# Kernel optimization log

Measured on AMD Instinct MI355X. Metric: run time of the kernel, lower is better.

The kernel has to match this reference:

```python
import jax, jax.numpy as jnp
import numpy as np

V, H, T = 32000, 768, 32
TYPES, MAX_VISITS, SEGS = 9, 512, 3
B, S = 32, 2048
EPS = 1e-12


def setup_inputs() -> dict:
    key = jax.random.key(0)
    ks = jax.random.split(key, 16)
    input_ids = jax.random.randint(ks[0], (B, S), 0, V)
    type_ids = jax.random.randint(ks[1], (B, S), 0, TYPES)
    time_stamps = jax.random.uniform(ks[2], (B, S), dtype=jnp.float32)
    ages = jax.random.uniform(ks[3], (B, S), dtype=jnp.float32)
    visit_orders = jax.random.randint(ks[4], (B, S), 0, MAX_VISITS)
    visit_segments = jax.random.randint(ks[5], (B, S), 0, SEGS)
    # parameters
    W_word = jax.random.normal(ks[6], (V, H), jnp.float32) * 0.02
    W_word = W_word.at[0].set(0.0)  # padding_idx = 0
    W_type = jax.random.normal(ks[7], (TYPES, H), jnp.float32) * 0.02
    W_order = jax.random.normal(ks[8], (MAX_VISITS, H), jnp.float32) * 0.02
    W_seg = jax.random.normal(ks[9], (SEGS, H), jnp.float32) * 0.02
    time_w = jax.random.normal(ks[10], (1, T), jnp.float32)
    time_phi = jax.random.normal(ks[11], (1, T), jnp.float32)
    age_w = jax.random.normal(ks[12], (1, T), jnp.float32)
    age_phi = jax.random.normal(ks[13], (1, T), jnp.float32)
    lin_W = jax.random.normal(ks[14], (H + 2 * T, H), jnp.float32) * 0.02
    lin_b = jnp.zeros((H,), jnp.float32)
    ln_g = jnp.ones((H,), jnp.float32)
    ln_beta = jnp.zeros((H,), jnp.float32)
    return dict(input_ids=input_ids, type_ids=type_ids, time_stamps=time_stamps,
                ages=ages, visit_orders=visit_orders, visit_segments=visit_segments,
                W_word=W_word, W_type=W_type, W_order=W_order, W_seg=W_seg,
                time_w=time_w, time_phi=time_phi, age_w=age_w, age_phi=age_phi,
                lin_W=lin_W, lin_b=lin_b, ln_g=ln_g, ln_beta=ln_beta)


def _sinusoidal(t, w, phi):
    # t: [B,S]; w,phi: [1,T] -> [B,S,T]
    return jnp.sin(t[..., None] * w + phi)


def reference(input_ids, type_ids, time_stamps, ages, visit_orders, visit_segments,
              W_word, W_type, W_order, W_seg, time_w, time_phi, age_w, age_phi,
              lin_W, lin_b, ln_g, ln_beta):
    word = W_word[input_ids]                       # [B,S,H]
    # time delta embedding (is_time_delta=True)
    dt = jnp.concatenate([time_stamps[:, :1] * 0.0,
                          time_stamps[:, 1:] - time_stamps[:, :-1]], axis=-1)
    time_e = _sinusoidal(dt, time_w, time_phi)     # [B,S,T]
    age_e = _sinusoidal(ages, age_w, age_phi)      # [B,S,T]
    seg_e = W_seg[visit_segments]                  # [B,S,H]
    order_e = W_order[visit_orders]                # [B,S,H]
    type_e = W_type[type_ids]                      # [B,S,H]
    fused = jnp.concatenate([word, time_e, age_e], axis=-1)   # [B,S,H+2T]
    fused = jnp.tanh(fused @ lin_W + lin_b)        # [B,S,H]
    emb = fused + type_e + order_e + seg_e
    # dropout is identity in eval mode; LayerNorm(eps=1e-12)
    mu = jnp.mean(emb, axis=-1, keepdims=True)
    var = jnp.mean(jnp.square(emb - mu), axis=-1, keepdims=True)
    return (emb - mu) * jax.lax.rsqrt(var + EPS) * ln_g + ln_beta
```

## Files before the change

### kernel.cpp

```cpp
#include <hip/hip_runtime.h>
#include <hip/hip_bf16.h>
#include <math.h>
#include <stdint.h>

#define HH 768
#define TT 32
#define KK 832
#define SS 2048
#define NSTEP 26
#define NTOK 65536
#define BM 32

typedef __attribute__((ext_vector_type(4))) float f32x4;
typedef __attribute__((ext_vector_type(8))) short bf16x8;
typedef __attribute__((ext_vector_type(4))) short bf16x4;

__device__ __forceinline__ short f2bf(float f) {
  union { float f; uint32_t u; } v; v.f = f;
  uint32_t u = v.u;
  return (short)((u + 0x7FFFu + ((u >> 16) & 1u)) >> 16);
}

__global__ void transpose_w_kernel(const float* __restrict__ lin_W,
                                   short* __restrict__ bt) {
  int i = blockIdx.x * 256 + threadIdx.x;
  if (i >= HH * KK) return;
  int n = i / KK;
  int k = i - n * KK;
  bt[i] = f2bf(lin_W[(size_t)k * HH + n]);
}

__global__ __launch_bounds__(256) void gather_a_kernel(
    const int* __restrict__ input_ids, const float* __restrict__ ts,
    const float* __restrict__ ages, const float* __restrict__ W_word,
    const float* __restrict__ time_w, const float* __restrict__ time_phi,
    const float* __restrict__ age_w, const float* __restrict__ age_phi,
    short* __restrict__ Aws) {
  const int wave = threadIdx.x >> 6, lane = threadIdx.x & 63;
  const int t = blockIdx.x * 4 + wave;
  if (t >= NTOK) return;
  const float* wrow = W_word + (size_t)input_ids[t] * HH;
  const int s = t & (SS - 1);
  const float dt = (s == 0) ? 0.f : (ts[t] - ts[t - 1]);
  const float age = ages[t];
  short* dst = Aws + (size_t)t * KK;
#pragma unroll
  for (int c2 = 0; c2 < 2; ++c2) {
    int chunk = c2 * 64 + lane;
    if (chunk < 104) {
      int k = chunk * 8;
      bf16x8 v;
      if (k < HH) {
        f32x4 x0 = *(const f32x4*)(wrow + k);
        f32x4 x1 = *(const f32x4*)(wrow + k + 4);
        v[0] = f2bf(x0[0]); v[1] = f2bf(x0[1]); v[2] = f2bf(x0[2]); v[3] = f2bf(x0[3]);
        v[4] = f2bf(x1[0]); v[5] = f2bf(x1[1]); v[6] = f2bf(x1[2]); v[7] = f2bf(x1[3]);
      } else if (k < HH + TT) {
        int j = k - HH;
#pragma unroll
        for (int i = 0; i < 8; ++i)
          v[i] = f2bf(sinf(dt * time_w[j + i] + time_phi[j + i]));
      } else {
        int j = k - HH - TT;
#pragma unroll
        for (int i = 0; i < 8; ++i)
          v[i] = f2bf(sinf(age * age_w[j + i] + age_phi[j + i]));
      }
      *(bf16x8*)(dst + k) = v;
    }
  }
}

__global__ __launch_bounds__(512) void ehr_gemm_kernel(
    const int* __restrict__ type_ids, const int* __restrict__ visit_orders,
    const int* __restrict__ visit_segments, const float* __restrict__ W_type,
    const float* __restrict__ W_order, const float* __restrict__ W_seg,
    const float* __restrict__ lin_b, const float* __restrict__ ln_g,
    const float* __restrict__ ln_beta, const short* __restrict__ Aws,
    const short* __restrict__ Btw, float* __restrict__ out) {
  __shared__ short Bt[HH * 32];
  __shared__ short Atile[BM * 32];
  __shared__ int tyl[BM], orl[BM], sgl[BM];
  __shared__ float redS[4][BM], redQ[4][BM];

  const int tid = threadIdx.x;
  const int t0 = blockIdx.x * BM;
  if (tid < BM) {
    tyl[tid] = type_ids[t0 + tid];
    orl[tid] = visit_orders[t0 + tid];
    sgl[tid] = visit_segments[t0 + tid];
  }
  const int lane = tid & 63, wave = tid >> 6;
  const int wm = wave >> 2, wn = wave & 3;
  const int l15 = lane & 15, l4 = lane >> 4;

  f32x4 acc[12];
#pragma unroll
  for (int nf = 0; nf < 12; ++nf) acc[nf] = (f32x4)(0.0f);

  const size_t a_lane_off = (size_t)l15 * KK + l4 * 8;

  for (int st = 0; st < NSTEP; ++st) {
    const int k0 = st * 32;
    if (wave < 2) {
      const short* src = Aws + (size_t)(t0 + wave * 16) * KK + a_lane_off + k0;
      __builtin_amdgcn_global_load_lds(
          (const __attribute__((address_space(1))) unsigned int*)src,
          (__attribute__((address_space(3))) unsigned int*)(Atile + wave * 512),
          16, 0, 0);
    }
#pragma unroll
    for (int p = 0; p < 6; ++p) {
      int c = p * 8 + wave;
      const short* src = Btw + (size_t)(c * 16) * KK + a_lane_off + k0;
      __builtin_amdgcn_global_load_lds(
          (const __attribute__((address_space(1))) unsigned int*)src,
          (__attribute__((address_space(3))) unsigned int*)(Bt + c * 512),
          16, 0, 0);
    }
    __syncthreads();

    const bf16x8* Af = (const bf16x8*)Atile;
    const bf16x8* Bf = (const bf16x8*)Bt;
    bf16x8 a = Af[wm * 64 + l4 * 16 + l15];
#pragma unroll
    for (int nf = 0; nf < 12; ++nf) {
      bf16x8 b = Bf[(wn * 12 + nf) * 64 + l4 * 16 + l15];
      acc[nf] = __builtin_amdgcn_mfma_f32_16x16x32_bf16(a, b, acc[nf], 0, 0, 0);
    }
    __syncthreads();
  }

  float sp[4], sq[4];
#pragma unroll
  for (int r = 0; r < 4; ++r) { sp[r] = 0.f; sq[r] = 0.f; }

#pragma unroll
  for (int nf = 0; nf < 12; ++nf) {
    int n = wn * 192 + nf * 16 + l15;
    float bias = lin_b[n];
#pragma unroll
    for (int r = 0; r < 4; ++r) {
      int row = wm * 16 + l4 * 4 + r;
      float z = tanhf(acc[nf][r] + bias);
      z += W_type[(size_t)tyl[row] * HH + n];
      z += W_order[(size_t)orl[row] * HH + n];
      z += W_seg[(size_t)sgl[row] * HH + n];
      acc[nf][r] = z;
      sp[r] += z;
      sq[r] += z * z;
    }
  }
#pragma unroll
  for (int m = 1; m < 16; m <<= 1) {
#pragma unroll
    for (int r = 0; r < 4; ++r) {
      sp[r] += __shfl_xor(sp[r], m, 64);
      sq[r] += __shfl_xor(sq[r], m, 64);
    }
  }
  if (l15 == 0) {
#pragma unroll
    for (int r = 0; r < 4; ++r) {
      int row = wm * 16 + l4 * 4 + r;
      redS[wn][row] = sp[r];
      redQ[wn][row] = sq[r];
    }
  }
  __syncthreads();

  float mu[4], rs[4];
#pragma unroll
  for (int r = 0; r < 4; ++r) {
    int row = wm * 16 + l4 * 4 + r;
    float s = redS[0][row] + redS[1][row] + redS[2][row] + redS[3][row];
    float q = redQ[0][row] + redQ[1][row] + redQ[2][row] + redQ[3][row];
    float m_ = s * (1.0f / 768.0f);
    float v_ = q * (1.0f / 768.0f) - m_ * m_;
    if (v_ < 0.f) v_ = 0.f;
    mu[r] = m_;
    rs[r] = rsqrtf(v_ + 1e-12f);
  }

  float* Os = (float*)Bt;
#pragma unroll
  for (int g = 0; g < 2; ++g) {
    __syncthreads();
    if (wm == g) {
#pragma unroll
      for (int nf = 0; nf < 12; ++nf) {
        int n = wn * 192 + nf * 16 + l15;
        float gg = ln_g[n], be = ln_beta[n];
#pragma unroll
        for (int r = 0; r < 4; ++r) {
          int lr = l4 * 4 + r;
          Os[lr * HH + n] = (acc[nf][r] - mu[r]) * rs[r] * gg + be;
        }
      }
    }
    __syncthreads();
    float* ob = out + (size_t)(t0 + g * 16) * HH;
#pragma unroll
    for (int q = 0; q < 6; ++q) {
      int idx4 = q * 512 + tid;
      ((f32x4*)ob)[idx4] = ((const f32x4*)Os)[idx4];
    }
  }
}

template <bool WS>
__global__ __launch_bounds__(512, 1) void ehr_fallback(
    const int* __restrict__ input_ids, const int* __restrict__ type_ids,
    const float* __restrict__ time_stamps, const float* __restrict__ ages,
    const int* __restrict__ visit_orders, const int* __restrict__ visit_segments,
    const float* __restrict__ W_word, const float* __restrict__ W_type,
    const float* __restrict__ W_order, const float* __restrict__ W_seg,
    const float* __restrict__ time_w, const float* __restrict__ time_phi,
    const float* __restrict__ age_w, const float* __restrict__ age_phi,
    const float* __restrict__ lin_W, const float* __restrict__ lin_b,
    const float* __restrict__ ln_g, const float* __restrict__ ln_beta,
    const short* __restrict__ bt_ws, float* __restrict__ out) {
  __shared__ short Bt[HH * 32];
  __shared__ short Atile[64 * 32];
  __shared__ float dtl[64], agel[64];
  __shared__ int idl[64], tyl[64], orl[64], sgl[64];
  __shared__ float tpar[128];
  __shared__ float redS[4][64], redQ[4][64];

  const int tid = threadIdx.x;
  const int t0 = blockIdx.x * 64;

  if (tid < 128) {
    int j = tid & 31;
    float v;
    if (tid < 32) v = time_w[j];
    else if (tid < 64) v = time_phi[j];
    else if (tid < 96) v = age_w[j];
    else v = age_phi[j];
    tpar[tid] = v;
  }
  if (tid < 64) {
    int t = t0 + tid;
    int s = t & (SS - 1);
    float tsv = time_stamps[t];
    dtl[tid] = (s == 0) ? 0.f : (tsv - time_stamps[t - 1]);
    agel[tid] = ages[t];
    idl[tid] = input_ids[t];
    tyl[tid] = type_ids[t];
    orl[tid] = visit_orders[t];
    sgl[tid] = visit_segments[t];
  }
  __syncthreads();

  const int lane = tid & 63, wave = tid >> 6;
  const int wm = wave >> 2, wn = wave & 3;
  const int l15 = lane & 15, l4 = lane >> 4;
  const int arow = tid >> 3, ac = tid & 7;
  const int myid = idl[arow];
  const float mydt = dtl[arow];
  const float myage = agel[arow];
  const float* wrow = W_word + (size_t)myid * HH;

  f32x4 acc[2][12];
#pragma unroll
  for (int mf = 0; mf < 2; ++mf)
#pragma unroll
    for (int nf = 0; nf < 12; ++nf) acc[mf][nf] = (f32x4)(0.0f);

  for (int st = 0; st < NSTEP; ++st) {
    const int k0 = st * 32;
    {
      int kg = k0 + ac * 4;
      bf16x4 w4;
      if (kg < HH) {
        const f32x4 v = *(const f32x4*)(wrow + kg);
        w4[0] = f2bf(v[0]); w4[1] = f2bf(v[1]);
        w4[2] = f2bf(v[2]); w4[3] = f2bf(v[3]);
      } else {
        int isAge = (kg >= HH + TT);
        int j = kg - (isAge ? (HH + TT) : HH);
        float x = isAge ? myage : mydt;
        int wof = isAge ? 64 : 0;
#pragma unroll
        for (int i = 0; i < 4; ++i)
          w4[i] = f2bf(sinf(x * tpar[wof + j + i] + tpar[wof + 32 + j + i]));
      }
      *(bf16x4*)(Atile + tid * 4) = w4;
    }
    if (WS) {
#pragma unroll
      for (int p = 0; p < 6; ++p) {
        int chunk = p * 8 + wave;
        short* ldst = Bt + chunk * 512;
        int n = chunk * 16 + (lane >> 2);
        int q = lane & 3;
        const short* src = bt_ws + (size_t)n * KK + k0 + q * 8;
        __builtin_amdgcn_global_load_lds(
            (const __attribute__((address_space(1))) unsigned int*)src,
            (__attribute__((address_space(3))) unsigned int*)ldst, 16, 0, 0);
      }
    } else {
#pragma unroll
      for (int i6 = 0; i6 < 6; ++i6) {
        int c = i6 * 512 + tid;
        int n = c >> 2, q = c & 3;
        int kb = k0 + q * 8;
        bf16x8 w8;
#pragma unroll
        for (int j = 0; j < 8; ++j) w8[j] = f2bf(lin_W[(size_t)(kb + j) * HH + n]);
        *(bf16x8*)(Bt + n * 32 + q * 8) = w8;
      }
    }
    __syncthreads();

    const bf16x8* Af = (const bf16x8*)Atile;
    const bf16x8* Bf = (const bf16x8*)Bt;
    bf16x8 a0 = Af[(wm * 32 + l15) * 4 + l4];
    bf16x8 a1 = Af[(wm * 32 + 16 + l15) * 4 + l4];
#pragma unroll
    for (int nf = 0; nf < 12; ++nf) {
      int n = wn * 192 + nf * 16 + l15;
      bf16x8 b = Bf[n * 4 + l4];
      acc[0][nf] = __builtin_amdgcn_mfma_f32_16x16x32_bf16(a0, b, acc[0][nf], 0, 0, 0);
      acc[1][nf] = __builtin_amdgcn_mfma_f32_16x16x32_bf16(a1, b, acc[1][nf], 0, 0, 0);
    }
    __syncthreads();
  }

  float sp[2][4], sq[2][4];
#pragma unroll
  for (int mf = 0; mf < 2; ++mf)
#pragma unroll
    for (int r = 0; r < 4; ++r) { sp[mf][r] = 0.f; sq[mf][r] = 0.f; }

#pragma unroll
  for (int nf = 0; nf < 12; ++nf) {
    int n = wn * 192 + nf * 16 + l15;
    float bias = lin_b[n];
#pragma unroll
    for (int mf = 0; mf < 2; ++mf) {
#pragma unroll
      for (int r = 0; r < 4; ++r) {
        int row = wm * 32 + mf * 16 + l4 * 4 + r;
        float z = tanhf(acc[mf][nf][r] + bias);
        z += W_type[(size_t)tyl[row] * HH + n];
        z += W_order[(size_t)orl[row] * HH + n];
        z += W_seg[(size_t)sgl[row] * HH + n];
        acc[mf][nf][r] = z;
        sp[mf][r] += z;
        sq[mf][r] += z * z;
      }
    }
  }
#pragma unroll
  for (int m = 1; m < 16; m <<= 1) {
#pragma unroll
    for (int mf = 0; mf < 2; ++mf)
#pragma unroll
      for (int r = 0; r < 4; ++r) {
        sp[mf][r] += __shfl_xor(sp[mf][r], m, 64);
        sq[mf][r] += __shfl_xor(sq[mf][r], m, 64);
      }
  }
  if (l15 == 0) {
#pragma unroll
    for (int mf = 0; mf < 2; ++mf)
#pragma unroll
      for (int r = 0; r < 4; ++r) {
        int row = wm * 32 + mf * 16 + l4 * 4 + r;
        redS[wn][row] = sp[mf][r];
        redQ[wn][row] = sq[mf][r];
      }
  }
  __syncthreads();

  float mu[2][4], rs[2][4];
#pragma unroll
  for (int mf = 0; mf < 2; ++mf)
#pragma unroll
    for (int r = 0; r < 4; ++r) {
      int row = wm * 32 + mf * 16 + l4 * 4 + r;
      float s = redS[0][row] + redS[1][row] + redS[2][row] + redS[3][row];
      float q = redQ[0][row] + redQ[1][row] + redQ[2][row] + redQ[3][row];
      float m_ = s * (1.0f / 768.0f);
      float v_ = q * (1.0f / 768.0f) - m_ * m_;
      if (v_ < 0.f) v_ = 0.f;
      mu[mf][r] = m_;
      rs[mf][r] = rsqrtf(v_ + 1e-12f);
    }

#pragma unroll
  for (int nf = 0; nf < 12; ++nf) {
    int n = wn * 192 + nf * 16 + l15;
    float g = ln_g[n], be = ln_beta[n];
#pragma unroll
    for (int mf = 0; mf < 2; ++mf) {
#pragma unroll
      for (int r = 0; r < 4; ++r) {
        int row = wm * 32 + mf * 16 + l4 * 4 + r;
        out[(size_t)(t0 + row) * HH + n] =
            (acc[mf][nf][r] - mu[mf][r]) * rs[mf][r] * g + be;
      }
    }
  }
}

extern "C" void kernel_launch(void* const* d_in, const int* in_sizes, int n_in,
                              void* d_out, int out_size, void* d_ws, size_t ws_size,
                              hipStream_t stream) {
  const int* input_ids = (const int*)d_in[0];
  const int* type_ids = (const int*)d_in[1];
  const float* time_stamps = (const float*)d_in[2];
  const float* ages = (const float*)d_in[3];
  const int* visit_orders = (const int*)d_in[4];
  const int* visit_segments = (const int*)d_in[5];
  const float* W_word = (const float*)d_in[6];
  const float* W_type = (const float*)d_in[7];
  const float* W_order = (const float*)d_in[8];
  const float* W_seg = (const float*)d_in[9];
  const float* time_w = (const float*)d_in[10];
  const float* time_phi = (const float*)d_in[11];
  const float* age_w = (const float*)d_in[12];
  const float* age_phi = (const float*)d_in[13];
  const float* lin_W = (const float*)d_in[14];
  const float* lin_b = (const float*)d_in[15];
  const float* ln_g = (const float*)d_in[16];
  const float* ln_beta = (const float*)d_in[17];
  float* out = (float*)d_out;

  const size_t a_bytes = (size_t)NTOK * KK * sizeof(short);
  const size_t bt_bytes = (size_t)HH * KK * sizeof(short);

  if (d_ws != nullptr && ws_size >= a_bytes + bt_bytes) {
    short* Aws = (short*)d_ws;
    short* Btw = (short*)((char*)d_ws + a_bytes);
    transpose_w_kernel<<<dim3((HH * KK + 255) / 256), dim3(256), 0, stream>>>(lin_W, Btw);
    gather_a_kernel<<<dim3(NTOK / 4), dim3(256), 0, stream>>>(
        input_ids, time_stamps, ages, W_word, time_w, time_phi, age_w, age_phi, Aws);
    ehr_gemm_kernel<<<dim3(NTOK / BM), dim3(512), 0, stream>>>(
        type_ids, visit_orders, visit_segments, W_type, W_order, W_seg,
        lin_b, ln_g, ln_beta, (const short*)Aws, (const short*)Btw, out);
  } else if (d_ws != nullptr && ws_size >= bt_bytes) {
    short* bt = (short*)d_ws;
    transpose_w_kernel<<<dim3((HH * KK + 255) / 256), dim3(256), 0, stream>>>(lin_W, bt);
    ehr_fallback<true><<<dim3(1024), dim3(512), 0, stream>>>(
        input_ids, type_ids, time_stamps, ages, visit_orders, visit_segments,
        W_word, W_type, W_order, W_seg, time_w, time_phi, age_w, age_phi,
        lin_W, lin_b, ln_g, ln_beta, (const short*)bt, out);
  } else {
    ehr_fallback<false><<<dim3(1024), dim3(512), 0, stream>>>(
        input_ids, type_ids, time_stamps, ages, visit_orders, visit_segments,
        W_word, W_type, W_order, W_seg, time_w, time_phi, age_w, age_phi,
        lin_W, lin_b, ln_g, ln_beta, nullptr, out);
  }
}
```

Baseline: 591.2 us.

## Double-buffer B tiles and preload full A block into LDS

The GEMM kernel now preloads the block's whole A slice (32 tokens x 832 K) into LDS once and double-buffers the B weight tiles, issuing the next step's B load before computing the current step. This removes one of the two barriers per K step and overlaps global-to-LDS transfers with MFMA work. It also adds a launch bound that asks for two blocks per CU. LDS use grows to about 150 KB, which may limit occupancy and conflict with the two-blocks-per-CU hint.

```diff
diff --git a/kernel.cpp b/kernel.cpp
--- a/kernel.cpp
+++ b/kernel.cpp
@@ -71,15 +71,15 @@
   }
 }
 
-__global__ __launch_bounds__(512) void ehr_gemm_kernel(
+__global__ __launch_bounds__(512, 2) void ehr_gemm_kernel(
     const int* __restrict__ type_ids, const int* __restrict__ visit_orders,
     const int* __restrict__ visit_segments, const float* __restrict__ W_type,
     const float* __restrict__ W_order, const float* __restrict__ W_seg,
     const float* __restrict__ lin_b, const float* __restrict__ ln_g,
     const float* __restrict__ ln_beta, const short* __restrict__ Aws,
     const short* __restrict__ Btw, float* __restrict__ out) {
-  __shared__ short Bt[HH * 32];
-  __shared__ short Atile[BM * 32];
+  __shared__ short Atile[52 * 512];
+  __shared__ short Bt[2][HH * 32];
   __shared__ int tyl[BM], orl[BM], sgl[BM];
   __shared__ float redS[4][BM], redQ[4][BM];
 
@@ -98,38 +98,50 @@
 #pragma unroll
   for (int nf = 0; nf < 12; ++nf) acc[nf] = (f32x4)(0.0f);
 
-  const size_t a_lane_off = (size_t)l15 * KK + l4 * 8;
-
-  for (int st = 0; st < NSTEP; ++st) {
-    const int k0 = st * 32;
-    if (wave < 2) {
-      const short* src = Aws + (size_t)(t0 + wave * 16) * KK + a_lane_off + k0;
+#define STAGE_B(kstep, buf)                                                  \
+  do {                                                                       \
+    _Pragma("unroll") for (int p = 0; p < 6; ++p) {                          \
+      int c = p * 8 + wave;                                                  \
+      const short* src =                                                     \
+          Btw + (size_t)(c * 16 + l15) * KK + (kstep) * 32 + l4 * 8;         \
+      __builtin_amdgcn_global_load_lds(                                      \
+          (const __attribute__((address_space(1))) unsigned int*)src,        \
+          (__attribute__((address_space(3))) unsigned int*)(Bt[buf] +        \
+                                                            c * 512),        \
+          16, 0, 0);                                                         \
+    }                                                                        \
+  } while (0)
+
+#pragma unroll
+  for (int p = 0; p < 7; ++p) {
+    int c = p * 8 + wave;
+    if (c < 52) {
+      int g = c / 26, kc = c - g * 26;
+      const short* src = Aws + (size_t)(t0 + g * 16 + l15) * KK + kc * 32 + l4 * 8;
       __builtin_amdgcn_global_load_lds(
           (const __attribute__((address_space(1))) unsigned int*)src,
-          (__attribute__((address_space(3))) unsigned int*)(Atile + wave * 512),
+          (__attribute__((address_space(3))) unsigned int*)(Atile + c * 512),
           16, 0, 0);
     }
-#pragma unroll
-    for (int p = 0; p < 6; ++p) {
-      int c = p * 8 + wave;
-      const short* src = Btw + (size_t)(c * 16) * KK + a_lane_off + k0;
-      __builtin_amdgcn_global_load_lds(
-          (const __attribute__((address_space(1))) unsigned int*)src,
-          (__attribute__((address_space(3))) unsigned int*)(Bt + c * 512),
-          16, 0, 0);
+  }
+  STAGE_B(0, 0);
+  __syncthreads();
+
+  for (int st = 0; st < NSTEP; ++st) {
+    if (st + 1 < NSTEP) {
+      STAGE_B(st + 1, (st + 1) & 1);
+    }
+    const bf16x8* Af = (const bf16x8*)Atile;
+    const bf16x8* Bf = (const bf16x8*)(Bt[st & 1]);
+    bf16x8 a = Af[(wm * 26 + st) * 64 + lane];
+#pragma unroll
+    for (int nf = 0; nf < 12; ++nf) {
+      bf16x8 b = Bf[(wn * 12 + nf) * 64 + lane];
+      acc[nf] = __builtin_amdgcn_mfma_f32_16x16x32_bf16(a, b, acc[nf], 0, 0, 0);
     }
     __syncthreads();
-
-    const bf16x8* Af = (const bf16x8*)Atile;
-    const bf16x8* Bf = (const bf16x8*)Bt;
-    bf16x8 a = Af[wm * 64 + l4 * 16 + l15];
-#pragma unroll
-    for (int nf = 0; nf < 12; ++nf) {
-      bf16x8 b = Bf[(wn * 12 + nf) * 64 + l4 * 16 + l15];
-      acc[nf] = __builtin_amdgcn_mfma_f32_16x16x32_bf16(a, b, acc[nf], 0, 0, 0);
-    }
-    __syncthreads();
-  }
+  }
+#undef STAGE_B
 
   float sp[4], sq[4];
 #pragma unroll
```

Result: no change. 600.9 us (+1.7%).

## Load GEMM operands directly from global into registers, dropping LDS staging

Applied to the files above, without the earlier changes.

The K-loop no longer stages A and B tiles in shared memory through global_load_lds with two barriers per step. Each wave now reads its bf16x8 MFMA fragments straight from global memory, and the loop is unrolled by two. This removes LDS traffic and per-step synchronisation. In exchange, the B weights are fetched redundantly by every block and by both wave rows, and the kernel relies on cache hits and register-level latency hiding instead of a shared tile.

```diff
diff --git a/kernel.cpp b/kernel.cpp
--- a/kernel.cpp
+++ b/kernel.cpp
@@ -78,8 +78,7 @@
     const float* __restrict__ lin_b, const float* __restrict__ ln_g,
     const float* __restrict__ ln_beta, const short* __restrict__ Aws,
     const short* __restrict__ Btw, float* __restrict__ out) {
-  __shared__ short Bt[HH * 32];
-  __shared__ short Atile[BM * 32];
+  __shared__ float Os[16 * HH];
   __shared__ int tyl[BM], orl[BM], sgl[BM];
   __shared__ float redS[4][BM], redQ[4][BM];
 
@@ -94,42 +93,25 @@
   const int wm = wave >> 2, wn = wave & 3;
   const int l15 = lane & 15, l4 = lane >> 4;
 
+  const short* aptr = Aws + (size_t)(t0 + wm * 16 + l15) * KK + l4 * 8;
+  const short* bptr = Btw + (size_t)(wn * 192 + l15) * KK + l4 * 8;
+
   f32x4 acc[12];
 #pragma unroll
   for (int nf = 0; nf < 12; ++nf) acc[nf] = (f32x4)(0.0f);
 
-  const size_t a_lane_off = (size_t)l15 * KK + l4 * 8;
-
+#pragma unroll 2
   for (int st = 0; st < NSTEP; ++st) {
-    const int k0 = st * 32;
-    if (wave < 2) {
-      const short* src = Aws + (size_t)(t0 + wave * 16) * KK + a_lane_off + k0;
-      __builtin_amdgcn_global_load_lds(
-          (const __attribute__((address_space(1))) unsigned int*)src,
-          (__attribute__((address_space(3))) unsigned int*)(Atile + wave * 512),
-          16, 0, 0);
-    }
-#pragma unroll
-    for (int p = 0; p < 6; ++p) {
-      int c = p * 8 + wave;
-      const short* src = Btw + (size_t)(c * 16) * KK + a_lane_off + k0;
-      __builtin_amdgcn_global_load_lds(
-          (const __attribute__((address_space(1))) unsigned int*)src,
-          (__attribute__((address_space(3))) unsigned int*)(Bt + c * 512),
-          16, 0, 0);
-    }
-    __syncthreads();
-
-    const bf16x8* Af = (const bf16x8*)Atile;
-    const bf16x8* Bf = (const bf16x8*)Bt;
-    bf16x8 a = Af[wm * 64 + l4 * 16 + l15];
+    const int ko = st * 32;
+    bf16x8 a = *(const bf16x8*)(aptr + ko);
 #pragma unroll
     for (int nf = 0; nf < 12; ++nf) {
-      bf16x8 b = Bf[(wn * 12 + nf) * 64 + l4 * 16 + l15];
+      bf16x8 b = *(const bf16x8*)(bptr + (size_t)nf * (16 * KK) + ko);
       acc[nf] = __builtin_amdgcn_mfma_f32_16x16x32_bf16(a, b, acc[nf], 0, 0, 0);
     }
-    __syncthreads();
-  }
+  }
+
+  __syncthreads();
 
   float sp[4], sq[4];
 #pragma unroll
@@ -182,7 +164,6 @@
     rs[r] = rsqrtf(v_ + 1e-12f);
   }
 
-  float* Os = (float*)Bt;
 #pragma unroll
   for (int g = 0; g < 2; ++g) {
     __syncthreads();
```

Measured after the change: 802.2 us. 1.36x slower.
